# Kernel optimization log

Measured on AMD Instinct MI355X. Metric: run time of the kernel, lower is better.

## Reference

```python
import jax, jax.numpy as jnp
import numpy as np

NUM_HEADS = 12


def setup_inputs() -> dict:
    key = jax.random.key(0)
    ks = jax.random.split(key, 10)
    B, S, H = 4, 1024, 768
    hd = H // NUM_HEADS
    hk = hv = 64
    scale = 1.0 / np.sqrt(H)
    inp = {
        "hidden_states": jax.random.normal(ks[0], (B, S, H), dtype=jnp.float32),
        "attention_mask": jnp.ones((B, S), dtype=jnp.float32),
        "Wq": jax.random.normal(ks[1], (H, H), dtype=jnp.float32) * scale,
        "bq": jnp.zeros((H,), dtype=jnp.float32),
        "Wk": jax.random.normal(ks[2], (H, H), dtype=jnp.float32) * scale,
        "bk": jnp.zeros((H,), dtype=jnp.float32),
        "Wv": jax.random.normal(ks[3], (H, H), dtype=jnp.float32) * scale,
        "bv": jnp.zeros((H,), dtype=jnp.float32),
        "E_key": jax.random.normal(ks[4], (2 * hk + 1, hd), dtype=jnp.float32) * 0.02,
        "E_val": jax.random.normal(ks[5], (2 * hv + 1, hd), dtype=jnp.float32) * 0.02,
    }
    return inp


def reference(hidden_states, attention_mask, Wq, bq, Wk, bk, Wv, bv, E_key, E_val):
    B, S, H = hidden_states.shape
    hd = H // NUM_HEADS

    def split_heads(x):  # [B,S,H] -> [B,nh,S,hd]
        return x.reshape(B, S, NUM_HEADS, hd).transpose(0, 2, 1, 3)

    q = split_heads(hidden_states @ Wq + bq)
    k = split_heads(hidden_states @ Wk + bk)
    v = split_heads(hidden_states @ Wv + bv)

    # content scores (note: original code applies NO 1/sqrt(d) scaling)
    scores = jnp.einsum("bhid,bhjd->bhij", q, k)

    # relative key-position scores: scores_pos[i,j] = q_i . E_key[j-i+hk] (banded)
    Rk = E_key.shape[0]
    hk = (Rk - 1) // 2
    rel = jnp.arange(S)[None, :] - jnp.arange(S)[:, None] + hk  # [S,S]
    valid_k = (rel >= 0) & (rel < Rk)
    p = jnp.einsum("bhid,rd->bhir", q, E_key)  # [B,nh,S,Rk]
    rel_c = jnp.clip(rel, 0, Rk - 1)
    scores_pos = jnp.take_along_axis(p, rel_c[None, None, :, :], axis=-1)
    scores = scores + jnp.where(valid_k[None, None], scores_pos, 0.0)

    # attention mask: (1 - m) * finfo.min added to scores
    ext = (1.0 - attention_mask[:, None, None, :]) * jnp.finfo(scores.dtype).min
    probs = jax.nn.softmax(scores + ext, axis=-1)

    ctx = jnp.einsum("bhij,bhjd->bhid", probs, v)

    # relative value-position: ctx_pos[i] = sum_j probs[i,j] * E_val[j-i+hv]
    Rv = E_val.shape[0]
    hv = (Rv - 1) // 2
    j_idx = jnp.arange(S)[:, None] + jnp.arange(Rv)[None, :] - hv  # [S,Rv]
    valid_v = (j_idx >= 0) & (j_idx < S)
    j_c = jnp.clip(j_idx, 0, S - 1)
    probs_band = jnp.take_along_axis(probs, j_c[None, None, :, :], axis=-1)
    probs_band = probs_band * valid_v[None, None].astype(probs.dtype)
    ctx = ctx + jnp.einsum("bhir,rd->bhid", probs_band, E_val)

    return ctx.transpose(0, 2, 1, 3).reshape(B, S, H)
```

## Files before the change

### kernel.cpp

```cpp
#include <hip/hip_runtime.h>
#include <hip/hip_bf16.h>
#include <math.h>

#define NH 12
#define SEQ 1024
#define HD 64
#define HDIM 768
#define BSZ 4
#define RK 129
#define FMIN -3.4028234663852886e38f
#define LOG2E 1.4426950408889634f

typedef __attribute__((ext_vector_type(8))) short short8;
typedef __attribute__((ext_vector_type(4))) short short4v;
typedef __attribute__((ext_vector_type(2))) unsigned uint2v;
typedef __attribute__((ext_vector_type(8))) _Float16 f16x8;
typedef __attribute__((ext_vector_type(4))) float f32x4;

__device__ inline short f2bf(float x) {
    union { __hip_bfloat16 h; short s; } u;
    u.h = __float2bfloat16(x);
    return u.s;
}
__device__ inline unsigned cvtpk(float lo, float hi) {
    unsigned r;
    asm("v_cvt_pk_bf16_f32 %0, %1, %2" : "=v"(r) : "v"(lo), "v"(hi));
    return r;
}
__device__ inline float fexp2(float x) {
    float r;
    asm("v_exp_f32 %0, %1" : "=v"(r) : "v"(x));
    return r;
}

__device__ inline void async_load16(void* lds, const void* g) {
    __builtin_amdgcn_global_load_lds(
        (const __attribute__((address_space(1))) unsigned int*)g,
        (__attribute__((address_space(3))) unsigned int*)lds, 16, 0, 0);
}

#define BAR()      asm volatile("s_barrier" ::: "memory")
#define WAITV0()   asm volatile("s_waitcnt vmcnt(0)" ::: "memory")
#define WAITLGKM() do { asm volatile("s_waitcnt lgkmcnt(0)" ::: "memory"); \
                        __builtin_amdgcn_sched_barrier(0); } while (0)

#define NXCHUNK 393216
#define NECHUNK 1032
#define NEVCHUNK 1280
#define NCONVB ((NXCHUNK + NECHUNK + NEVCHUNK + 255) / 256)
#define NTRB   (144 * 3)
__global__ __launch_bounds__(256) void prep_kernel(
    const float* __restrict__ X, const float* __restrict__ Ek,
    const float* __restrict__ Ev,
    const float* __restrict__ Wq, const float* __restrict__ Wk, const float* __restrict__ Wv,
    _Float16* __restrict__ Xh, _Float16* __restrict__ Ekh, short* __restrict__ Evt,
    _Float16* __restrict__ Wtq, _Float16* __restrict__ Wtk, _Float16* __restrict__ Wtv)
{
    const int bidg = blockIdx.x;
    if (bidg < NCONVB) {
        int idx = bidg * 256 + threadIdx.x;
        if (idx < NXCHUNK + NECHUNK) {
            const float* src;
            _Float16* dst;
            if (idx < NXCHUNK) { src = X; dst = Xh; }
            else { idx -= NXCHUNK; src = Ek; dst = Ekh; }
            float4 a = ((const float4*)src)[idx * 2];
            float4 b = ((const float4*)src)[idx * 2 + 1];
            f16x8 o;
            o[0] = (_Float16)a.x; o[1] = (_Float16)a.y; o[2] = (_Float16)a.z; o[3] = (_Float16)a.w;
            o[4] = (_Float16)b.x; o[5] = (_Float16)b.y; o[6] = (_Float16)b.z; o[7] = (_Float16)b.w;
            ((f16x8*)dst)[idx] = o;
        } else if (idx < NXCHUNK + NECHUNK + NEVCHUNK) {
            idx -= NXCHUNK + NECHUNK;
            const int dim = idx / 20;
            const int r0  = (idx % 20) * 8;
            short8 o;
#pragma unroll
            for (int e = 0; e < 8; ++e) {
                int rel = r0 + e;
                float v = (rel < RK) ? Ev[(size_t)rel * HD + dim] : 0.0f;
                o[e] = f2bf(v);
            }
            *(short8*)&Evt[(size_t)dim * 160 + r0] = o;
        }
        return;
    }
    const int bid2 = bidg - NCONVB;
    const int z = bid2 / 144;
    const int r = bid2 % 144;
    const float* __restrict__ W = (z == 0) ? Wq : (z == 1) ? Wk : Wv;
    _Float16* __restrict__ Wt   = (z == 0) ? Wtq : (z == 1) ? Wtk : Wtv;

    __shared__ float sT[64][65];
    const int t  = threadIdx.x;
    const int k0 = (r / 12) * 64;
    const int n0 = (r % 12) * 64;

    const int c  = (t & 15) * 4;
    const int kr = t >> 4;
#pragma unroll
    for (int rr = 0; rr < 4; ++rr) {
        float4 v = *(const float4*)&W[(size_t)(k0 + kr + rr * 16) * HDIM + n0 + c];
        sT[c + 0][kr + rr * 16] = v.x;
        sT[c + 1][kr + rr * 16] = v.y;
        sT[c + 2][kr + rr * 16] = v.z;
        sT[c + 3][kr + rr * 16] = v.w;
    }
    __syncthreads();
    const int rn = t >> 2;
    const int ck = (t & 3) * 16;
#pragma unroll
    for (int g = 0; g < 2; ++g) {
        f16x8 o;
#pragma unroll
        for (int e = 0; e < 8; ++e) o[e] = (_Float16)sT[rn][ck + g * 8 + e];
        *(f16x8*)&Wt[(size_t)(n0 + rn) * HDIM + k0 + ck + g * 8] = o;
    }
}

__global__ __launch_bounds__(256) void qkv_mfma_kernel(
    const _Float16* __restrict__ Xh,
    const _Float16* __restrict__ Wtq, const _Float16* __restrict__ Wtk, const _Float16* __restrict__ Wtv,
    const float* __restrict__ bq, const float* __restrict__ bk, const float* __restrict__ bv,
    _Float16* __restrict__ Qo, _Float16* __restrict__ Ko, short* __restrict__ Vt)
{
    int bid = blockIdx.x;
    bid = (bid & 7) * 72 + (bid >> 3);
    const int which = bid / 192;
    const int rem   = bid % 192;
    const int n0    = (rem / 32) * 128;
    const int m0    = (rem % 32) * 128;
    const _Float16* __restrict__ Wt = (which == 0) ? Wtq : (which == 1) ? Wtk : Wtv;
    const float* __restrict__ bias  = (which == 0) ? bq : (which == 1) ? bk : bv;
    const float qscale = (which == 0) ? LOG2E : 1.0f;

    __shared__ __align__(16) _Float16 sA[128 * 64];
    __shared__ __align__(16) _Float16 sB[128 * 64];

    const int t  = threadIdx.x;
    const int w  = t >> 6, l = t & 63;
    const int lq = l & 15, lg = l >> 4;
    const int wr = w >> 1, wc = w & 1;

    f32x4 acc[4][4];
#pragma unroll
    for (int i = 0; i < 4; ++i)
#pragma unroll
        for (int j = 0; j < 4; ++j) acc[i][j] = (f32x4){0.f, 0.f, 0.f, 0.f};

    for (int k0 = 0; k0 < HDIM; k0 += 64) {
        __syncthreads();
#pragma unroll
        for (int r = 0; r < 4; ++r) {
            const int cib = r * 256 + w * 64;
            const int ci  = cib + l;
            const int row = ci >> 3, cr = ci & 7;
            const int lc  = cr ^ (row & 7);
            async_load16(&sA[(size_t)cib * 8],
                         &Xh[(size_t)(m0 + row) * HDIM + k0 + lc * 8]);
            async_load16(&sB[(size_t)cib * 8],
                         &Wt[(size_t)(n0 + row) * HDIM + k0 + lc * 8]);
        }
        __syncthreads();

        f16x8 af[4][2], bf[4][2];
#pragma unroll
        for (int i = 0; i < 4; ++i) {
#pragma unroll
            for (int ks = 0; ks < 2; ++ks) {
                int ra = wr * 64 + i * 16 + lq;
                af[i][ks] = *(const f16x8*)((const char*)sA +
                            ra * 128 + ((ks * 64 + lg * 16) ^ ((ra & 7) << 4)));
                int rb = wc * 64 + i * 16 + lq;
                bf[i][ks] = *(const f16x8*)((const char*)sB +
                            rb * 128 + ((ks * 64 + lg * 16) ^ ((rb & 7) << 4)));
            }
        }
#pragma unroll
        for (int i = 0; i < 4; ++i)
#pragma unroll
            for (int j = 0; j < 4; ++j) {
                acc[i][j] = __builtin_amdgcn_mfma_f32_16x16x32_f16(af[i][0], bf[j][0], acc[i][j], 0, 0, 0);
                acc[i][j] = __builtin_amdgcn_mfma_f32_16x16x32_f16(af[i][1], bf[j][1], acc[i][j], 0, 0, 0);
            }
    }

    _Float16* __restrict__ Yh = (which == 0) ? Qo : Ko;
#pragma unroll
    for (int i = 0; i < 4; ++i) {
        const int mb = m0 + wr * 64 + i * 16 + lg * 4;
        const int bb = mb >> 10, ss = mb & 1023;
#pragma unroll
        for (int j = 0; j < 4; ++j) {
            const int n  = n0 + wc * 64 + j * 16 + lq;
            const float bv4 = bias[n];
            const int hh = n >> 6, dd = n & 63;
            if (which == 2) {
                short4v pk;
#pragma unroll
                for (int reg = 0; reg < 4; ++reg)
                    pk[reg] = f2bf(acc[i][j][reg] + bv4);
                *(short4v*)&Vt[((size_t)(bb * NH + hh) * HD + dd) * SEQ + ss] = pk;
            } else {
#pragma unroll
                for (int reg = 0; reg < 4; ++reg) {
                    const size_t off = ((size_t)(bb * NH + hh) * SEQ + ss + reg) * HD + dd;
                    Yh[off] = (_Float16)((acc[i][j][reg] + bv4) * qscale);
                }
            }
        }
    }
}

__global__ __launch_bounds__(256, 3) void attn_mfma_kernel(
    const _Float16* __restrict__ Q, const _Float16* __restrict__ K,
    const short* __restrict__ Vt, const float* __restrict__ mask,
    const _Float16* __restrict__ Ekh, const short* __restrict__ Evt,
    float* __restrict__ out)
{
    __shared__ __align__(16) char smem[41984];
    float* sMt = (float*)(smem + 37888);

    int bid = blockIdx.x;
    bid = (bid & 7) * 96 + (bid >> 3);
    const int bh = bid >> 4;
    const int i0 = (bid & 15) * 64;
    const int b  = bh / NH;
    const int h  = bh - b * NH;

    const int t  = threadIdx.x;
    const int w  = t >> 6;
    const int l  = t & 63;
    const int lq = l & 15;
    const int lg = l >> 4;
    const int wrow0 = i0 + w * 16;
    const int bt0 = __builtin_amdgcn_readfirstlane(((wrow0 - 64 + 1024) >> 5) - 32);

    const int krow = t >> 3, klc = (t & 7) ^ (krow & 7);
    const int vrow = t >> 2, vlc = (t & 3) ^ ((vrow >> 1) & 3);
    const _Float16* Ksrc = K + ((size_t)bh * SEQ + krow) * HD + klc * 8;
    const short*    Vsrc = Vt + ((size_t)bh * HD + vrow) * SEQ + vlc * 8;

    const _Float16* qp = Q + ((size_t)bh * SEQ + wrow0 + lq) * HD;
    f16x8 qf0 = *(const f16x8*)&qp[lg * 8];
    f16x8 qf1 = *(const f16x8*)&qp[32 + lg * 8];

    _Float16* povl = (_Float16*)(smem + 16384 + w * 4224);
#pragma unroll
    for (int nt = 0; nt < 9; ++nt) {
        int cc = nt * 16 + lq;
        f16x8 eb0 = {0, 0, 0, 0, 0, 0, 0, 0};
        f16x8 eb1 = {0, 0, 0, 0, 0, 0, 0, 0};
        if (cc < RK) {
            eb0 = *(const f16x8*)&Ekh[(size_t)cc * HD + lg * 8];
            eb1 = *(const f16x8*)&Ekh[(size_t)cc * HD + 32 + lg * 8];
        }
        f32x4 pc = {0.f, 0.f, 0.f, 0.f};
        pc = __builtin_amdgcn_mfma_f32_16x16x32_f16(qf0, eb0, pc, 0, 0, 0);
        pc = __builtin_amdgcn_mfma_f32_16x16x32_f16(qf1, eb1, pc, 0, 0, 0);
        if (cc < RK) {
#pragma unroll
            for (int reg = 0; reg < 4; ++reg)
                povl[(lg * 4 + reg) * 132 + cc] = (_Float16)pc[reg];
        }
    }
    float ppos[5][2][4];
#pragma unroll
    for (int s = 0; s < 5; ++s) {
        const int jts = bt0 + s;
#pragma unroll
        for (int ct = 0; ct < 2; ++ct)
#pragma unroll
            for (int reg = 0; reg < 4; ++reg) {
                const int rel = jts * 32 + ct * 16 + lg * 4 + reg - wrow0 - lq + 64;
                float v = 0.f;
                if ((unsigned)jts < 32u && (unsigned)rel < (unsigned)RK)
                    v = (float)povl[lq * 132 + rel];
                ppos[s][ct][reg] = v;
            }
    }

    {
        float4 mv = *(const float4*)&mask[(size_t)b * SEQ + t * 4];
        float4 mo;
        mo.x = ((1.0f - mv.x) * FMIN) * LOG2E;
        mo.y = ((1.0f - mv.y) * FMIN) * LOG2E;
        mo.z = ((1.0f - mv.z) * FMIN) * LOG2E;
        mo.w = ((1.0f - mv.w) * FMIN) * LOG2E;
        *(float4*)&sMt[t * 4] = mo;
    }

    WAITLGKM();
    BAR();

    async_load16(smem + t * 16,          Ksrc);
    async_load16(smem + 16384 + t * 16,  Vsrc);
    async_load16(smem + 4096 + t * 16,   Ksrc + 32 * HD);
    async_load16(smem + 20480 + t * 16,  Vsrc + 32);
    WAITV0();
    BAR();

    f32x4 acc[4];
#pragma unroll
    for (int nt = 0; nt < 4; ++nt) acc[nt] = (f32x4){0.f, 0.f, 0.f, 0.f};
    f32x4 zacc = {0.f, 0.f, 0.f, 0.f};

    const short8 ones = {0x3F80, 0x3F80, 0x3F80, 0x3F80,
                         0x3F80, 0x3F80, 0x3F80, 0x3F80};

    unsigned band[5][2][2];
#pragma unroll
    for (int s = 0; s < 5; ++s)
#pragma unroll
        for (int ct = 0; ct < 2; ++ct) { band[s][ct][0] = 0u; band[s][ct][1] = 0u; }

    const int ck0 = ((lg ^ (lq & 7)) << 4);
    const int ck1 = (((4 + lg) ^ (lq & 7)) << 4);
    char* sPw = smem + 32768 + w * 1280;
    const int vslot = (lg ^ ((lq >> 1) & 3)) << 4;

    auto do_subtile = [&](int jtc) {
        char* bK = smem + (jtc & 3) * 4096;
        char* bV = smem + 16384 + (jtc & 3) * 4096;
        const int j0c = jtc * 32;
        f32x4 sc[2];
#pragma unroll
        for (int ct = 0; ct < 2; ++ct) {
            const int rb = (ct * 16 + lq) * 128;
            f16x8 kb0 = *(const f16x8*)(bK + rb + ck0);
            f16x8 kb1 = *(const f16x8*)(bK + rb + ck1);
            f32x4 s = {0.f, 0.f, 0.f, 0.f};
            s = __builtin_amdgcn_mfma_f32_16x16x32_f16(kb0, qf0, s, 0, 0, 0);
            s = __builtin_amdgcn_mfma_f32_16x16x32_f16(kb1, qf1, s, 0, 0, 0);
            sc[ct] = s;
        }
        float p[2][4];
        if ((unsigned)(jtc - bt0) < 5u) {
#pragma unroll
            for (int s = 0; s < 5; ++s) {
                if (jtc == bt0 + s) {
#pragma unroll
                    for (int ct = 0; ct < 2; ++ct) {
                        f32x4 mtv = *(const f32x4*)&sMt[j0c + ct * 16 + lg * 4];
#pragma unroll
                        for (int reg = 0; reg < 4; ++reg)
                            p[ct][reg] = fexp2(sc[ct][reg] + mtv[reg] + ppos[s][ct][reg]);
                        band[s][ct][0] = cvtpk(p[ct][0], p[ct][1]);
                        band[s][ct][1] = cvtpk(p[ct][2], p[ct][3]);
                    }
                }
            }
        } else {
#pragma unroll
            for (int ct = 0; ct < 2; ++ct) {
                f32x4 mtv = *(const f32x4*)&sMt[j0c + ct * 16 + lg * 4];
#pragma unroll
                for (int reg = 0; reg < 4; ++reg)
                    p[ct][reg] = fexp2(sc[ct][reg] + mtv[reg]);
            }
        }
#pragma unroll
        for (int ct = 0; ct < 2; ++ct) {
            uint2v pw;
            pw[0] = cvtpk(p[ct][0], p[ct][1]);
            pw[1] = cvtpk(p[ct][2], p[ct][3]);
            *(uint2v*)(sPw + lq * 80 + ct * 32 + lg * 8) = pw;
        }
        short8 pa = *(const short8*)(sPw + lq * 80 + lg * 16);
        zacc = __builtin_amdgcn_mfma_f32_16x16x32_bf16(pa, ones, zacc, 0, 0, 0);
#pragma unroll
        for (int nt = 0; nt < 4; ++nt) {
            short8 vb = *(const short8*)(bV + (nt * 16 + lq) * 64 + vslot);
            acc[nt] = __builtin_amdgcn_mfma_f32_16x16x32_bf16(pa, vb, acc[nt], 0, 0, 0);
        }
    };

    for (int j = 0; j < 16; ++j) {
        if (j < 15) {
            const int jn = 2 * j + 2;
            async_load16(smem + (jn & 3) * 4096 + t * 16,
                         Ksrc + (size_t)jn * 32 * HD);
            async_load16(smem + 16384 + (jn & 3) * 4096 + t * 16,
                         Vsrc + jn * 32);
            async_load16(smem + ((jn + 1) & 3) * 4096 + t * 16,
                         Ksrc + (size_t)(jn + 1) * 32 * HD);
            async_load16(smem + 16384 + ((jn + 1) & 3) * 4096 + t * 16,
                         Vsrc + (jn + 1) * 32);
        }

        do_subtile(2 * j);
        do_subtile(2 * j + 1);

        WAITV0();
        BAR();
    }

    char* bandLds = smem + w * 5120;
    {
        short8 z8 = {0, 0, 0, 0, 0, 0, 0, 0};
#pragma unroll
        for (int i = 0; i < 5; ++i)
            *(short8*)(bandLds + l * 16 + i * 1024) = z8;
    }
#pragma unroll
    for (int s = 0; s < 5; ++s) {
        const int jts = bt0 + s;
        if ((unsigned)jts < 32u) {
#pragma unroll
            for (int ct = 0; ct < 2; ++ct)
#pragma unroll
                for (int hh = 0; hh < 2; ++hh) {
                    const unsigned pw = band[s][ct][hh];
                    const int k0v  = jts * 32 + ct * 16 + lg * 4 + hh * 2;
                    const int rel0 = k0v - wrow0 - lq + 64;
                    if ((unsigned)rel0 < (unsigned)RK)
                        *(short*)(bandLds + lq * 320 + rel0 * 2) = (short)(pw & 0xffff);
                    if ((unsigned)(rel0 + 1) < (unsigned)RK)
                        *(short*)(bandLds + lq * 320 + rel0 * 2 + 2) = (short)(pw >> 16);
                }
        }
    }

    short8 bandA[5];
#pragma unroll
    for (int ks = 0; ks < 5; ++ks)
        bandA[ks] = *(const short8*)(bandLds + lq * 320 + ks * 64 + lg * 16);
#pragma unroll
    for (int nt = 0; nt < 4; ++nt) {
#pragma unroll
        for (int ks = 0; ks < 5; ++ks) {
            short8 eb = *(const short8*)&Evt[(size_t)(nt * 16 + lq) * 160 + ks * 32 + lg * 8];
            acc[nt] = __builtin_amdgcn_mfma_f32_16x16x32_bf16(bandA[ks], eb, acc[nt], 0, 0, 0);
        }
    }

#pragma unroll
    for (int nt = 0; nt < 4; ++nt) {
#pragma unroll
        for (int reg = 0; reg < 4; ++reg) {
            int qi = wrow0 + lg * 4 + reg;
            out[((size_t)b * SEQ + qi) * HDIM + h * HD + nt * 16 + lq] =
                acc[nt][reg] / zacc[reg];
        }
    }
}

extern "C" void kernel_launch(void* const* d_in, const int* in_sizes, int n_in,
                              void* d_out, int out_size, void* d_ws, size_t ws_size,
                              hipStream_t stream) {
    const float* X    = (const float*)d_in[0];
    const float* mask = (const float*)d_in[1];
    const float* Wq   = (const float*)d_in[2];
    const float* bq   = (const float*)d_in[3];
    const float* Wk   = (const float*)d_in[4];
    const float* bk   = (const float*)d_in[5];
    const float* Wv   = (const float*)d_in[6];
    const float* bv   = (const float*)d_in[7];
    const float* Ek   = (const float*)d_in[8];
    const float* Ev   = (const float*)d_in[9];
    float* out        = (float*)d_out;

    char* ws = (char*)d_ws;
    const size_t SZ_QKV = (size_t)BSZ * NH * SEQ * HD * 2;
    const size_t SZ_W   = (size_t)HDIM * HDIM * 2;
    _Float16* Qh  = (_Float16*)(ws);
    _Float16* Kh  = (_Float16*)(ws + SZ_QKV);
    short*    Vt  = (short*)   (ws + 2 * SZ_QKV);
    _Float16* Xh  = (_Float16*)(ws + 3 * SZ_QKV);
    _Float16* Wtq = (_Float16*)(ws + 4 * SZ_QKV);
    _Float16* Wtk = (_Float16*)(ws + 4 * SZ_QKV + SZ_W);
    _Float16* Wtv = (_Float16*)(ws + 4 * SZ_QKV + 2 * SZ_W);
    _Float16* Ekh = (_Float16*)(ws + 4 * SZ_QKV + 3 * SZ_W);
    short*    Evt = (short*)   (ws + 4 * SZ_QKV + 3 * SZ_W + 20480);

    prep_kernel<<<NCONVB + NTRB, 256, 0, stream>>>(
        X, Ek, Ev, Wq, Wk, Wv, Xh, Ekh, Evt, Wtq, Wtk, Wtv);
    qkv_mfma_kernel<<<576, 256, 0, stream>>>(Xh, Wtq, Wtk, Wtv, bq, bk, bv, Qh, Kh, Vt);
    attn_mfma_kernel<<<768, 256, 0, stream>>>(Qh, Kh, Vt, mask, Ekh, Evt, out);
}
```

Baseline: 76.83 us.

## Load V fragments directly from global into registers instead of via LDS

V tiles, previously staged through shared memory with async copies, are now loaded straight from global memory into per-lane registers and prefetched one iteration ahead. Each wave loads its own copy of the V fragments. This shrinks shared memory from about 41KB to 25KB and removes the LDS reads for V, which could raise occupancy. In exchange it adds register pressure, since 16 short8 values are live across the loop, and the global V traffic is redundant because every wave fetches the same data.

```diff
diff --git a/kernel.cpp b/kernel.cpp
--- a/kernel.cpp
+++ b/kernel.cpp
@@ -218,8 +218,8 @@
     const _Float16* __restrict__ Ekh, const short* __restrict__ Evt,
     float* __restrict__ out)
 {
-    __shared__ __align__(16) char smem[41984];
-    float* sMt = (float*)(smem + 37888);
+    __shared__ __align__(16) char smem[25600];
+    float* sMt = (float*)(smem + 21504);
 
     int bid = blockIdx.x;
     bid = (bid & 7) * 96 + (bid >> 3);
@@ -237,15 +237,14 @@
     const int bt0 = __builtin_amdgcn_readfirstlane(((wrow0 - 64 + 1024) >> 5) - 32);
 
     const int krow = t >> 3, klc = (t & 7) ^ (krow & 7);
-    const int vrow = t >> 2, vlc = (t & 3) ^ ((vrow >> 1) & 3);
     const _Float16* Ksrc = K + ((size_t)bh * SEQ + krow) * HD + klc * 8;
-    const short*    Vsrc = Vt + ((size_t)bh * HD + vrow) * SEQ + vlc * 8;
+    const short* Vg = Vt + ((size_t)bh * HD + lq) * SEQ + lg * 8;
 
     const _Float16* qp = Q + ((size_t)bh * SEQ + wrow0 + lq) * HD;
     f16x8 qf0 = *(const f16x8*)&qp[lg * 8];
     f16x8 qf1 = *(const f16x8*)&qp[32 + lg * 8];
 
-    _Float16* povl = (_Float16*)(smem + 16384 + w * 4224);
+    _Float16* povl = (_Float16*)(smem + w * 4224);
 #pragma unroll
     for (int nt = 0; nt < 9; ++nt) {
         int cc = nt * 16 + lq;
@@ -293,10 +292,14 @@
     WAITLGKM();
     BAR();
 
-    async_load16(smem + t * 16,          Ksrc);
-    async_load16(smem + 16384 + t * 16,  Vsrc);
-    async_load16(smem + 4096 + t * 16,   Ksrc + 32 * HD);
-    async_load16(smem + 20480 + t * 16,  Vsrc + 32);
+    async_load16(smem + t * 16,         Ksrc);
+    async_load16(smem + 4096 + t * 16,  Ksrc + 32 * HD);
+    short8 vA[4], vB[4], nA[4], nB[4];
+#pragma unroll
+    for (int nt = 0; nt < 4; ++nt) {
+        vA[nt] = *(const short8*)(Vg + (size_t)nt * 16 * SEQ);
+        vB[nt] = *(const short8*)(Vg + (size_t)nt * 16 * SEQ + 32);
+    }
     WAITV0();
     BAR();
 
@@ -316,12 +319,10 @@
 
     const int ck0 = ((lg ^ (lq & 7)) << 4);
     const int ck1 = (((4 + lg) ^ (lq & 7)) << 4);
-    char* sPw = smem + 32768 + w * 1280;
-    const int vslot = (lg ^ ((lq >> 1) & 3)) << 4;
-
-    auto do_subtile = [&](int jtc) {
+    char* sPw = smem + 16384 + w * 1280;
+
+    auto do_subtile = [&](int jtc, const short8 vb[4]) {
         char* bK = smem + (jtc & 3) * 4096;
-        char* bV = smem + 16384 + (jtc & 3) * 4096;
         const int j0c = jtc * 32;
         f32x4 sc[2];
 #pragma unroll
@@ -369,10 +370,8 @@
         short8 pa = *(const short8*)(sPw + lq * 80 + lg * 16);
         zacc = __builtin_amdgcn_mfma_f32_16x16x32_bf16(pa, ones, zacc, 0, 0, 0);
 #pragma unroll
-        for (int nt = 0; nt < 4; ++nt) {
-            short8 vb = *(const short8*)(bV + (nt * 16 + lq) * 64 + vslot);
-            acc[nt] = __builtin_amdgcn_mfma_f32_16x16x32_bf16(pa, vb, acc[nt], 0, 0, 0);
-        }
+        for (int nt = 0; nt < 4; ++nt)
+            acc[nt] = __builtin_amdgcn_mfma_f32_16x16x32_bf16(pa, vb[nt], acc[nt], 0, 0, 0);
     };
 
     for (int j = 0; j < 16; ++j) {
@@ -380,19 +379,22 @@
             const int jn = 2 * j + 2;
             async_load16(smem + (jn & 3) * 4096 + t * 16,
                          Ksrc + (size_t)jn * 32 * HD);
-            async_load16(smem + 16384 + (jn & 3) * 4096 + t * 16,
-                         Vsrc + jn * 32);
             async_load16(smem + ((jn + 1) & 3) * 4096 + t * 16,
                          Ksrc + (size_t)(jn + 1) * 32 * HD);
-            async_load16(smem + 16384 + ((jn + 1) & 3) * 4096 + t * 16,
-                         Vsrc + (jn + 1) * 32);
-        }
-
-        do_subtile(2 * j);
-        do_subtile(2 * j + 1);
+#pragma unroll
+            for (int nt = 0; nt < 4; ++nt) {
+                nA[nt] = *(const short8*)(Vg + (size_t)nt * 16 * SEQ + jn * 32);
+                nB[nt] = *(const short8*)(Vg + (size_t)nt * 16 * SEQ + jn * 32 + 32);
+            }
+        }
+
+        do_subtile(2 * j, vA);
+        do_subtile(2 * j + 1, vB);
 
         WAITV0();
         BAR();
+#pragma unroll
+        for (int nt = 0; nt < 4; ++nt) { vA[nt] = nA[nt]; vB[nt] = nB[nt]; }
     }
 
     char* bandLds = smem + w * 5120;
```

Result: slower. 104.6 us (+36.2%).
